# Kernel tuning notes

Measured on AMD Instinct MI355X. Metric: run time of the kernel, lower is better.

## Reference

```python
import jax, jax.numpy as jnp
import numpy as np
from jax import lax

B, S, CIN, COUT, K = 32, 2048, 256, 256, 16


def setup_inputs() -> dict:
    key = jax.random.key(0)
    k1, k2, k3, k4 = jax.random.split(key, 4)
    x = jax.random.normal(k1, (B, S, CIN), dtype=jnp.float32)
    w_real = jax.random.normal(k2, (COUT, CIN, K), dtype=jnp.float32) * 0.1
    w_imag = jax.random.normal(k3, (COUT, CIN, K), dtype=jnp.float32) * 0.1
    phases = jax.random.normal(k4, (K,), dtype=jnp.float32) * 0.1
    return {"x": x, "w_real": w_real, "w_imag": w_imag, "phases": phases}


def reference(x, w_real, w_imag, phases):
    # out[b,t,o] = Re( sum_{k,i} x[b,t+k,i] * exp(1j*phases[k]) * (w_real + 1j*w_imag)[o,i,k] )
    # x is real, so this equals a real valid conv1d with effective kernel:
    #   w_eff[o,i,k] = cos(phases[k]) * w_real[o,i,k] - sin(phases[k]) * w_imag[o,i,k]
    w_eff = jnp.cos(phases)[None, None, :] * w_real - jnp.sin(phases)[None, None, :] * w_imag
    # conv expects NCH / OIH layouts
    y = lax.conv_general_dilated(
        jnp.transpose(x, (0, 2, 1)),  # [B, CIN, S]
        w_eff,                         # [COUT, CIN, K]
        window_strides=(1,),
        padding="VALID",
        dimension_numbers=("NCH", "OIH", "NCH"),
    )
    return jnp.transpose(y, (0, 2, 1))  # [B, S-K+1, COUT]
```

## Files before the change

kernel.cpp:

```cpp
#include <hip/hip_runtime.h>
#include <math.h>

#define B_    32
#define S_    2048
#define CIN_  256
#define COUT_ 256
#define K_    16
#define TOUT_ 2033
#define RTOT_ 4096

typedef __bf16 bf16x4 __attribute__((ext_vector_type(4)));
typedef __bf16 bf16x8 __attribute__((ext_vector_type(8)));
typedef float  f32x4  __attribute__((ext_vector_type(4)));

#define GLOBAL_AS __attribute__((address_space(1)))
#define LDS_AS    __attribute__((address_space(3)))

__device__ __forceinline__ void gload_lds16(const void* g, void* l) {
  __builtin_amdgcn_global_load_lds((const GLOBAL_AS void*)g, (LDS_AS void*)l, 16, 0, 0);
}

__global__ void __launch_bounds__(256) build_wt_kernel(const float* __restrict__ wr,
                                                       const float* __restrict__ wi,
                                                       const float* __restrict__ ph,
                                                       __bf16* __restrict__ wt) {
  int t = blockIdx.x * 256 + threadIdx.x;
  int o = t >> 8, i = t & 255;
  const float4* wr4 = (const float4*)(wr + (size_t)(o * CIN_ + i) * K_);
  const float4* wi4 = (const float4*)(wi + (size_t)(o * CIN_ + i) * K_);
  float re[16], im[16];
  #pragma unroll
  for (int v = 0; v < 4; v++) {
    float4 a = wr4[v];
    re[4*v+0]=a.x; re[4*v+1]=a.y; re[4*v+2]=a.z; re[4*v+3]=a.w;
    float4 b = wi4[v];
    im[4*v+0]=b.x; im[4*v+1]=b.y; im[4*v+2]=b.z; im[4*v+3]=b.w;
  }
  #pragma unroll
  for (int kk = 0; kk < K_; kk++) {
    float p = ph[kk];
    wt[(size_t)o * RTOT_ + kk * CIN_ + i] = (__bf16)(cosf(p)*re[kk] - sinf(p)*im[kk]);
  }
}

__global__ void __launch_bounds__(256) conv_mfma_kernel(const float* __restrict__ xg,
                                                        const __bf16* __restrict__ wt,
                                                        float* __restrict__ out) {
  __shared__ __align__(16) __bf16 As[144 * 32];
  __shared__ __align__(16) __bf16 Bs[128 * 32];

  const int bx = blockIdx.x;
  const int nb = bx & 1;
  const int mb = (bx >> 1) & 15;
  const int b  = bx >> 5;

  const int tid  = threadIdx.x;
  const int w    = tid >> 6;
  const int lane = tid & 63;
  const int wm   = w >> 1, wn = w & 1;
  const int n16  = lane & 15, q = lane >> 4;

  const int t0 = mb * 128;
  const int o0 = nb * 128;

  const float* xbase = xg + (size_t)b * (S_ * CIN_);

  const int sr = tid >> 3;
  const int sc = (tid & 7) * 4;
  const int br = w * 16 + (lane >> 2);
  const int bc = (lane & 3) * 8;

  f32x4 acc[4][4];
  #pragma unroll
  for (int im_ = 0; im_ < 4; im_++)
    #pragma unroll
    for (int in_ = 0; in_ < 4; in_++)
      acc[im_][in_] = {0.f, 0.f, 0.f, 0.f};

  for (int ic = 0; ic < 8; ++ic) {
    const int i0 = ic * 32;

    __syncthreads();

    {
      const float* xcol = xbase + i0 + sc;
      #pragma unroll
      for (int p = 0; p < 4; p++) {
        int r = p * 32 + sr;
        int rg = t0 + r; rg = (rg < S_) ? rg : (S_ - 1);
        float4 v = *(const float4*)(xcol + (size_t)rg * CIN_);
        bf16x4 o4; o4[0]=(__bf16)v.x; o4[1]=(__bf16)v.y; o4[2]=(__bf16)v.z; o4[3]=(__bf16)v.w;
        *(bf16x4*)(As + r * 32 + sc) = o4;
      }
      if (tid < 128) {
        int r = 128 + sr;
        int rg = t0 + r; rg = (rg < S_) ? rg : (S_ - 1);
        float4 v = *(const float4*)(xcol + (size_t)rg * CIN_);
        bf16x4 o4; o4[0]=(__bf16)v.x; o4[1]=(__bf16)v.y; o4[2]=(__bf16)v.z; o4[3]=(__bf16)v.w;
        *(bf16x4*)(As + r * 32 + sc) = o4;
      }
    }

    for (int kk = 0; kk < K_; ++kk) {
      if (kk) __syncthreads();

      const __bf16* wcol = wt + (size_t)kk * CIN_ + i0 + bc;
      #pragma unroll
      for (int p = 0; p < 2; p++) {
        int orow = o0 + p * 64 + br;
        gload_lds16(wcol + (size_t)orow * RTOT_,
                    (void*)(Bs + (p * 64 + w * 16) * 32));
      }

      __syncthreads();

      bf16x8 af[4], bfrag[4];
      #pragma unroll
      for (int jm = 0; jm < 4; jm++) {
        int row = kk + wm * 64 + jm * 16 + n16;
        af[jm] = *(const bf16x8*)(As + row * 32 + q * 8);
      }
      #pragma unroll
      for (int jn = 0; jn < 4; jn++) {
        int row = wn * 64 + jn * 16 + n16;
        bfrag[jn] = *(const bf16x8*)(Bs + row * 32 + q * 8);
      }
      #pragma unroll
      for (int jm = 0; jm < 4; jm++)
        #pragma unroll
        for (int jn = 0; jn < 4; jn++)
          acc[jm][jn] = __builtin_amdgcn_mfma_f32_16x16x32_bf16(af[jm], bfrag[jn], acc[jm][jn], 0, 0, 0);
    }
  }

  float* obase = out + (size_t)b * TOUT_ * COUT_;
  #pragma unroll
  for (int jm = 0; jm < 4; jm++) {
    #pragma unroll
    for (int r = 0; r < 4; r++) {
      int t = t0 + wm * 64 + jm * 16 + q * 4 + r;
      if (t < TOUT_) {
        float* orow = obase + (size_t)t * COUT_ + o0 + wn * 64 + n16;
        #pragma unroll
        for (int jn = 0; jn < 4; jn++)
          orow[jn * 16] = acc[jm][jn][r];
      }
    }
  }
}

extern "C" void kernel_launch(void* const* d_in, const int* in_sizes, int n_in,
                              void* d_out, int out_size, void* d_ws, size_t ws_size,
                              hipStream_t stream) {
  const float* x  = (const float*)d_in[0];
  const float* wr = (const float*)d_in[1];
  const float* wi = (const float*)d_in[2];
  const float* ph = (const float*)d_in[3];
  float* out = (float*)d_out;

  __bf16* wt = (__bf16*)d_ws;

  build_wt_kernel<<<dim3((COUT_ * CIN_) / 256), dim3(256), 0, stream>>>(wr, wi, ph, wt);
  conv_mfma_kernel<<<dim3(B_ * 16 * 2), dim3(256), 0, stream>>>(x, wt, out);
}
```

Before: 234.9 us.

## Switch conv GEMM to 32x32x16 MFMA with pre-swizzled weight layout

Replaces the 16x16x32 bf16 MFMA tiles with 32x32x16 MFMA tiles (2x2 per wave, split over two K-halves). The weight-building kernel now writes weights in a blocked layout so each kk/ic chunk is a contiguous 8 KB slab that can be loaded into LDS with coalesced 16-byte direct loads. The activation LDS tile becomes a k-group-major layout with padded row stride 145 to cut bank conflicts. The intent is fewer LDS fragment reads per FLOP and better global load coalescing, at the cost of a more complex indexing scheme.

```diff
diff --git a/kernel.cpp b/kernel.cpp
--- a/kernel.cpp
+++ b/kernel.cpp
@@ -11,7 +11,7 @@
 
 typedef __bf16 bf16x4 __attribute__((ext_vector_type(4)));
 typedef __bf16 bf16x8 __attribute__((ext_vector_type(8)));
-typedef float  f32x4  __attribute__((ext_vector_type(4)));
+typedef float  f32x16 __attribute__((ext_vector_type(16)));
 
 #define GLOBAL_AS __attribute__((address_space(1)))
 #define LDS_AS    __attribute__((address_space(3)))
@@ -36,18 +36,23 @@
     float4 b = wi4[v];
     im[4*v+0]=b.x; im[4*v+1]=b.y; im[4*v+2]=b.z; im[4*v+3]=b.w;
   }
+  const int ob = o >> 5, s = (i >> 4) & 1, kh = (i >> 3) & 1;
+  const int olow = o & 31, j = i & 7;
+  const int ic = i >> 5;
   #pragma unroll
   for (int kk = 0; kk < K_; kk++) {
     float p = ph[kk];
-    wt[(size_t)o * RTOT_ + kk * CIN_ + i] = (__bf16)(cosf(p)*re[kk] - sinf(p)*im[kk]);
+    int c = kk * 8 + ic;
+    int addr = (((c * 8 + ob) * 4 + s * 2 + kh) * 256) + olow * 8 + j;
+    wt[addr] = (__bf16)(cosf(p)*re[kk] - sinf(p)*im[kk]);
   }
 }
 
 __global__ void __launch_bounds__(256) conv_mfma_kernel(const float* __restrict__ xg,
                                                         const __bf16* __restrict__ wt,
                                                         float* __restrict__ out) {
-  __shared__ __align__(16) __bf16 As[144 * 32];
-  __shared__ __align__(16) __bf16 Bs[128 * 32];
+  __shared__ __align__(16) __bf16 As[4 * 145 * 8];
+  __shared__ __align__(16) __bf16 Bs[4096];
 
   const int bx = blockIdx.x;
   const int nb = bx & 1;
@@ -58,24 +63,27 @@
   const int w    = tid >> 6;
   const int lane = tid & 63;
   const int wm   = w >> 1, wn = w & 1;
-  const int n16  = lane & 15, q = lane >> 4;
+  const int l31  = lane & 31, lhi = lane >> 5;
 
   const int t0 = mb * 128;
   const int o0 = nb * 128;
 
-  const float* xbase = xg + (size_t)b * (S_ * CIN_);
+  const float*  xbase  = xg + (size_t)b * (S_ * CIN_);
+  const __bf16* wtbase = wt + nb * 4096;
 
   const int sr = tid >> 3;
   const int sc = (tid & 7) * 4;
-  const int br = w * 16 + (lane >> 2);
-  const int bc = (lane & 3) * 8;
+  const int sp = sc >> 3;
+  const int sj = sc & 7;
 
-  f32x4 acc[4][4];
+  f32x16 acc[2][2];
   #pragma unroll
-  for (int im_ = 0; im_ < 4; im_++)
+  for (int jm = 0; jm < 2; jm++)
     #pragma unroll
-    for (int in_ = 0; in_ < 4; in_++)
-      acc[im_][in_] = {0.f, 0.f, 0.f, 0.f};
+    for (int jn = 0; jn < 2; jn++)
+      #pragma unroll
+      for (int r = 0; r < 16; r++)
+        acc[jm][jn][r] = 0.f;
 
   for (int ic = 0; ic < 8; ++ic) {
     const int i0 = ic * 32;
@@ -90,60 +98,67 @@
         int rg = t0 + r; rg = (rg < S_) ? rg : (S_ - 1);
         float4 v = *(const float4*)(xcol + (size_t)rg * CIN_);
         bf16x4 o4; o4[0]=(__bf16)v.x; o4[1]=(__bf16)v.y; o4[2]=(__bf16)v.z; o4[3]=(__bf16)v.w;
-        *(bf16x4*)(As + r * 32 + sc) = o4;
+        *(bf16x4*)(As + (sp * 145 + r) * 8 + sj) = o4;
       }
       if (tid < 128) {
         int r = 128 + sr;
         int rg = t0 + r; rg = (rg < S_) ? rg : (S_ - 1);
         float4 v = *(const float4*)(xcol + (size_t)rg * CIN_);
         bf16x4 o4; o4[0]=(__bf16)v.x; o4[1]=(__bf16)v.y; o4[2]=(__bf16)v.z; o4[3]=(__bf16)v.w;
-        *(bf16x4*)(As + r * 32 + sc) = o4;
+        *(bf16x4*)(As + (sp * 145 + r) * 8 + sj) = o4;
       }
     }
 
     for (int kk = 0; kk < K_; ++kk) {
       if (kk) __syncthreads();
 
-      const __bf16* wcol = wt + (size_t)kk * CIN_ + i0 + bc;
+      const __bf16* gb = wtbase + (size_t)(kk * 8 + ic) * 8192;
       #pragma unroll
       for (int p = 0; p < 2; p++) {
-        int orow = o0 + p * 64 + br;
-        gload_lds16(wcol + (size_t)orow * RTOT_,
-                    (void*)(Bs + (p * 64 + w * 16) * 32));
+        int seg = w * 2 + p;
+        gload_lds16(gb + seg * 512 + lane * 8, (void*)(Bs + seg * 512));
       }
 
       __syncthreads();
 
-      bf16x8 af[4], bfrag[4];
+      bf16x8 af[2][2], bfr[2][2];
       #pragma unroll
-      for (int jm = 0; jm < 4; jm++) {
-        int row = kk + wm * 64 + jm * 16 + n16;
-        af[jm] = *(const bf16x8*)(As + row * 32 + q * 8);
-      }
+      for (int jm = 0; jm < 2; jm++)
+        #pragma unroll
+        for (int s = 0; s < 2; s++) {
+          int row = kk + wm * 64 + jm * 32 + l31;
+          af[jm][s] = *(const bf16x8*)(As + ((s * 2 + lhi) * 145 + row) * 8);
+        }
       #pragma unroll
-      for (int jn = 0; jn < 4; jn++) {
-        int row = wn * 64 + jn * 16 + n16;
-        bfrag[jn] = *(const bf16x8*)(Bs + row * 32 + q * 8);
-      }
+      for (int jn = 0; jn < 2; jn++)
+        #pragma unroll
+        for (int s = 0; s < 2; s++) {
+          int grp = (wn * 2 + jn) * 4 + s * 2 + lhi;
+          bfr[jn][s] = *(const bf16x8*)(Bs + grp * 256 + l31 * 8);
+        }
+
       #pragma unroll
-      for (int jm = 0; jm < 4; jm++)
+      for (int s = 0; s < 2; s++)
         #pragma unroll
-        for (int jn = 0; jn < 4; jn++)
-          acc[jm][jn] = __builtin_amdgcn_mfma_f32_16x16x32_bf16(af[jm], bfrag[jn], acc[jm][jn], 0, 0, 0);
+        for (int jm = 0; jm < 2; jm++)
+          #pragma unroll
+          for (int jn = 0; jn < 2; jn++)
+            acc[jm][jn] = __builtin_amdgcn_mfma_f32_32x32x16_bf16(af[jm][s], bfr[jn][s], acc[jm][jn], 0, 0, 0);
     }
   }
 
   float* obase = out + (size_t)b * TOUT_ * COUT_;
   #pragma unroll
-  for (int jm = 0; jm < 4; jm++) {
+  for (int jm = 0; jm < 2; jm++) {
     #pragma unroll
-    for (int r = 0; r < 4; r++) {
-      int t = t0 + wm * 64 + jm * 16 + q * 4 + r;
+    for (int reg = 0; reg < 16; reg++) {
+      int rowcd = (reg & 3) + 8 * (reg >> 2) + 4 * lhi;
+      int t = t0 + wm * 64 + jm * 32 + rowcd;
       if (t < TOUT_) {
-        float* orow = obase + (size_t)t * COUT_ + o0 + wn * 64 + n16;
+        float* orow = obase + (size_t)t * COUT_ + o0 + wn * 64 + l31;
         #pragma unroll
-        for (int jn = 0; jn < 4; jn++)
-          orow[jn * 16] = acc[jm][jn][r];
+        for (int jn = 0; jn < 2; jn++)
+          orow[jn * 32] = acc[jm][jn][reg];
       }
     }
   }
```

New measurement: 268.8 us. 1.14x slower.

## Load weight fragments directly to registers with prefetch, drop B LDS staging

Applied to the files above, without the earlier changes.

Weights are now pre-laid out in MFMA fragment order, so each lane loads its bf16x8 B fragments straight from global memory into registers. The next (kk, ic) step's fragments are double-buffered in registers while the current MFMAs run. This removes the B shared-memory tile and the two per-kk __syncthreads. The A tile row stride is padded to 36 to cut LDS bank conflicts. In exchange there are more global and L2 reads per wave, since fragments are no longer shared between waves through LDS, and higher register pressure.

```diff
diff --git a/kernel.cpp b/kernel.cpp
--- a/kernel.cpp
+++ b/kernel.cpp
@@ -7,18 +7,10 @@
 #define COUT_ 256
 #define K_    16
 #define TOUT_ 2033
-#define RTOT_ 4096
 
 typedef __bf16 bf16x4 __attribute__((ext_vector_type(4)));
 typedef __bf16 bf16x8 __attribute__((ext_vector_type(8)));
 typedef float  f32x4  __attribute__((ext_vector_type(4)));
-
-#define GLOBAL_AS __attribute__((address_space(1)))
-#define LDS_AS    __attribute__((address_space(3)))
-
-__device__ __forceinline__ void gload_lds16(const void* g, void* l) {
-  __builtin_amdgcn_global_load_lds((const GLOBAL_AS void*)g, (LDS_AS void*)l, 16, 0, 0);
-}
 
 __global__ void __launch_bounds__(256) build_wt_kernel(const float* __restrict__ wr,
                                                        const float* __restrict__ wi,
@@ -36,18 +28,23 @@
     float4 b = wi4[v];
     im[4*v+0]=b.x; im[4*v+1]=b.y; im[4*v+2]=b.z; im[4*v+3]=b.w;
   }
+  const int og = o >> 4, n = o & 15;
+  const int ic = i >> 5, q = (i >> 3) & 3, j = i & 7;
   #pragma unroll
   for (int kk = 0; kk < K_; kk++) {
     float p = ph[kk];
-    wt[(size_t)o * RTOT_ + kk * CIN_ + i] = (__bf16)(cosf(p)*re[kk] - sinf(p)*im[kk]);
+    int chunk = kk * 8 + ic;
+    wt[(size_t)chunk * 8192 + og * 512 + q * 128 + n * 8 + j]
+        = (__bf16)(cosf(p)*re[kk] - sinf(p)*im[kk]);
   }
 }
+
+#define AROW 36
 
 __global__ void __launch_bounds__(256) conv_mfma_kernel(const float* __restrict__ xg,
                                                         const __bf16* __restrict__ wt,
                                                         float* __restrict__ out) {
-  __shared__ __align__(16) __bf16 As[144 * 32];
-  __shared__ __align__(16) __bf16 Bs[128 * 32];
+  __shared__ __align__(16) __bf16 As[144 * AROW];
 
   const int bx = blockIdx.x;
   const int nb = bx & 1;
@@ -65,10 +62,10 @@
 
   const float* xbase = xg + (size_t)b * (S_ * CIN_);
 
+  const __bf16* wfrag = wt + (size_t)(nb * 8 + wn * 4) * 512 + lane * 8;
+
   const int sr = tid >> 3;
   const int sc = (tid & 7) * 4;
-  const int br = w * 16 + (lane >> 2);
-  const int bc = (lane & 3) * 8;
 
   f32x4 acc[4][4];
   #pragma unroll
@@ -76,6 +73,11 @@
     #pragma unroll
     for (int in_ = 0; in_ < 4; in_++)
       acc[im_][in_] = {0.f, 0.f, 0.f, 0.f};
+
+  bf16x8 bcur[4], bnext[4];
+  #pragma unroll
+  for (int jn = 0; jn < 4; jn++)
+    bcur[jn] = *(const bf16x8*)(wfrag + (size_t)jn * 512);
 
   for (int ic = 0; ic < 8; ++ic) {
     const int i0 = ic * 32;
@@ -90,46 +92,43 @@
         int rg = t0 + r; rg = (rg < S_) ? rg : (S_ - 1);
         float4 v = *(const float4*)(xcol + (size_t)rg * CIN_);
         bf16x4 o4; o4[0]=(__bf16)v.x; o4[1]=(__bf16)v.y; o4[2]=(__bf16)v.z; o4[3]=(__bf16)v.w;
-        *(bf16x4*)(As + r * 32 + sc) = o4;
+        *(bf16x4*)(As + r * AROW + sc) = o4;
       }
       if (tid < 128) {
         int r = 128 + sr;
         int rg = t0 + r; rg = (rg < S_) ? rg : (S_ - 1);
         float4 v = *(const float4*)(xcol + (size_t)rg * CIN_);
         bf16x4 o4; o4[0]=(__bf16)v.x; o4[1]=(__bf16)v.y; o4[2]=(__bf16)v.z; o4[3]=(__bf16)v.w;
-        *(bf16x4*)(As + r * 32 + sc) = o4;
+        *(bf16x4*)(As + r * AROW + sc) = o4;
       }
     }
 
+    __syncthreads();
+
     for (int kk = 0; kk < K_; ++kk) {
-      if (kk) __syncthreads();
+      int g  = ic * 16 + kk;
+      int gn = (g < 127) ? g + 1 : 127;
+      int chunk_n = ((gn & 15) << 3) + (gn >> 4);
+      #pragma unroll
+      for (int jn = 0; jn < 4; jn++)
+        bnext[jn] = *(const bf16x8*)(wfrag + (size_t)chunk_n * 8192 + (size_t)jn * 512);
 
-      const __bf16* wcol = wt + (size_t)kk * CIN_ + i0 + bc;
-      #pragma unroll
-      for (int p = 0; p < 2; p++) {
-        int orow = o0 + p * 64 + br;
-        gload_lds16(wcol + (size_t)orow * RTOT_,
-                    (void*)(Bs + (p * 64 + w * 16) * 32));
-      }
-
-      __syncthreads();
-
-      bf16x8 af[4], bfrag[4];
+      bf16x8 af[4];
       #pragma unroll
       for (int jm = 0; jm < 4; jm++) {
         int row = kk + wm * 64 + jm * 16 + n16;
-        af[jm] = *(const bf16x8*)(As + row * 32 + q * 8);
+        af[jm] = *(const bf16x8*)(As + row * AROW + q * 8);
       }
-      #pragma unroll
-      for (int jn = 0; jn < 4; jn++) {
-        int row = wn * 64 + jn * 16 + n16;
-        bfrag[jn] = *(const bf16x8*)(Bs + row * 32 + q * 8);
-      }
+
       #pragma unroll
       for (int jm = 0; jm < 4; jm++)
         #pragma unroll
         for (int jn = 0; jn < 4; jn++)
-          acc[jm][jn] = __builtin_amdgcn_mfma_f32_16x16x32_bf16(af[jm], bfrag[jn], acc[jm][jn], 0, 0, 0);
+          acc[jm][jn] = __builtin_amdgcn_mfma_f32_16x16x32_bf16(af[jm], bcur[jn], acc[jm][jn], 0, 0, 0);
+
+      #pragma unroll
+      for (int jn = 0; jn < 4; jn++)
+        bcur[jn] = bnext[jn];
     }
   }
 
```

New measurement: 237.4 us. Within noise of the previous version (+1.1%).
